# Performance work log

Measured on AMD Instinct MI355X. Metric: run time of the kernel, lower is better.

## Reference

```python
import jax, jax.numpy as jnp
import numpy as np

QLEN, MLEN, BSZ = 1024, 1024, 4
D_MODEL, N_HEAD, D_HEAD, D_INNER = 1024, 16, 64, 4096
KLEN = QLEN + MLEN  # = rlen
LN_EPS = 1e-5


def setup_inputs() -> dict:
    key = jax.random.key(0)
    ks = jax.random.split(key, 16)
    s = 0.02
    nhd = N_HEAD * D_HEAD
    inp = {
        "dec_inp": jax.random.normal(ks[0], (QLEN, BSZ, D_MODEL), jnp.float32),
        "r": jax.random.normal(ks[1], (KLEN, D_MODEL), jnp.float32),
        "r_w_bias": jax.random.normal(ks[2], (N_HEAD, D_HEAD), jnp.float32) * s,
        "r_r_bias": jax.random.normal(ks[3], (N_HEAD, D_HEAD), jnp.float32) * s,
        "mems": jax.random.normal(ks[4], (MLEN, BSZ, D_MODEL), jnp.float32),
        # causal mask with memory: position j visible to query i iff j <= i + MLEN
        "dec_attn_mask": (jnp.arange(KLEN)[None, :] > (jnp.arange(QLEN)[:, None] + MLEN))[:, :, None],
        # parameters
        "qkv_w": jax.random.normal(ks[5], (D_MODEL, 3 * nhd), jnp.float32) * s,
        "r_w": jax.random.normal(ks[6], (D_MODEL, nhd), jnp.float32) * s,
        "o_w": jax.random.normal(ks[7], (nhd, D_MODEL), jnp.float32) * s,
        "ln1_w": jnp.ones((D_MODEL,), jnp.float32),
        "ln1_b": jnp.zeros((D_MODEL,), jnp.float32),
        "ln2_w": jnp.ones((D_MODEL,), jnp.float32),
        "ln2_b": jnp.zeros((D_MODEL,), jnp.float32),
        "ff_w1": jax.random.normal(ks[8], (D_MODEL, D_INNER), jnp.float32) * s,
        "ff_b1": jnp.zeros((D_INNER,), jnp.float32),
        "ff_w2": jax.random.normal(ks[9], (D_INNER, D_MODEL), jnp.float32) * s,
        "ff_b2": jnp.zeros((D_MODEL,), jnp.float32),
    }
    return inp


def _layer_norm(x, w, b):
    mu = jnp.mean(x, axis=-1, keepdims=True)
    var = jnp.mean(jnp.square(x - mu), axis=-1, keepdims=True)
    return (x - mu) * jax.lax.rsqrt(var + LN_EPS) * w + b


def _rel_shift(x):
    # x: [qlen, rlen, bsz, n_head] -- Transformer-XL pad/reshape shift
    q, rl = x.shape[0], x.shape[1]
    zero_pad = jnp.zeros((q, 1) + x.shape[2:], x.dtype)
    x_padded = jnp.concatenate([zero_pad, x], axis=1)
    x_padded = x_padded.reshape((rl + 1, q) + x.shape[2:])
    return x_padded[1:].reshape(x.shape)


def reference(dec_inp, r, r_w_bias, r_r_bias, mems, dec_attn_mask,
              qkv_w, r_w, o_w, ln1_w, ln1_b, ln2_w, ln2_b,
              ff_w1, ff_b1, ff_w2, ff_b2):
    qlen, bsz = dec_inp.shape[0], dec_inp.shape[1]
    nhd = N_HEAD * D_HEAD
    scale = 1.0 / (D_HEAD ** 0.5)

    cat = jnp.concatenate([mems, dec_inp], axis=0)          # [klen, b, d]
    w_heads = cat @ qkv_w                                   # [klen, b, 3*nhd]
    w_head_q, w_head_k, w_head_v = jnp.split(w_heads, 3, axis=-1)
    w_head_q = w_head_q[-qlen:]                             # [qlen, b, nhd]
    klen = w_head_k.shape[0]

    w_head_q = w_head_q.reshape(qlen, bsz, N_HEAD, D_HEAD)
    w_head_k = w_head_k.reshape(klen, bsz, N_HEAD, D_HEAD)
    w_head_v = w_head_v.reshape(klen, bsz, N_HEAD, D_HEAD)
    r_head_k = (r @ r_w).reshape(-1, N_HEAD, D_HEAD)        # [rlen, n, d]

    AC = jnp.einsum('ibnd,jbnd->ijbn', w_head_q + r_w_bias, w_head_k)
    BD = jnp.einsum('ibnd,jnd->ijbn', w_head_q + r_r_bias, r_head_k)
    BD = _rel_shift(BD)

    attn_score = (AC + BD) * scale                          # [q, k, b, n]
    attn_score = jnp.where(dec_attn_mask[:, :, :, None], -jnp.inf, attn_score)
    attn_prob = jax.nn.softmax(attn_score, axis=1)

    attn_vec = jnp.einsum('ijbn,jbnd->ibnd', attn_prob, w_head_v)
    attn_out = attn_vec.reshape(qlen, bsz, nhd) @ o_w       # [q, b, d]

    output = _layer_norm(dec_inp + attn_out, ln1_w, ln1_b)
    ff = jax.nn.relu(output @ ff_w1 + ff_b1) @ ff_w2 + ff_b2
    return _layer_norm(output + ff, ln2_w, ln2_b)
```

## Files before the change

### kernel.cpp

```cpp
#include <hip/hip_runtime.h>
#include <hip/hip_bf16.h>
#include <math.h>

#define QLEN 1024
#define MLEN 1024
#define BSZ 4
#define KLEN 2048
#define NH 16
#define DH 64
#define DM 1024
#define DI 4096
#define NHD 1024
#define LN_EPS 1e-5f

typedef short bf16x8 __attribute__((ext_vector_type(8)));
typedef float f32x4 __attribute__((ext_vector_type(4)));
typedef unsigned int uint4v __attribute__((ext_vector_type(4)));

__device__ __forceinline__ float bf2f(unsigned short u) {
    union { unsigned u32; float f; } x; x.u32 = ((unsigned)u) << 16; return x.f;
}
__device__ __forceinline__ unsigned short f2bf(float f) {
    __hip_bfloat16 h = __float2bfloat16(f);
    return *(unsigned short*)&h;
}

static const size_t OFF_CATB  = 0;
static const size_t OFF_VTG   = 0;
static const size_t OFF_WHB   = 16777216;
static const size_t OFF_RB    = 67108864;
static const size_t OFF_RHKB  = 71303168;
static const size_t OFF_AVB   = 75497472;
static const size_t OFF_TMP   = 83886080;
static const size_t OFF_LN1F  = 100663296;
static const size_t OFF_LN1B  = 117440512;
static const size_t OFF_FFHB  = 125829120;
static const size_t OFF_QKVWT = 159383552;
static const size_t OFF_RWT   = 165675008;
static const size_t OFF_OWT   = 167772160;
static const size_t OFF_FFW1T = 169869312;
static const size_t OFF_FFW2T = 178257920;

__global__ __launch_bounds__(256) void cast_cat(const float* __restrict__ mems,
                                                const float* __restrict__ dec,
                                                unsigned short* __restrict__ out) {
    size_t i8 = ((size_t)blockIdx.x * 256 + threadIdx.x) * 8;
    const size_t half = (size_t)MLEN * BSZ * DM;
    const float* src = (i8 < half) ? (mems + i8) : (dec + (i8 - half));
    float4 v0 = *(const float4*)src;
    float4 v1 = *(const float4*)(src + 4);
    ushort4 o0 = {f2bf(v0.x), f2bf(v0.y), f2bf(v0.z), f2bf(v0.w)};
    ushort4 o1 = {f2bf(v1.x), f2bf(v1.y), f2bf(v1.z), f2bf(v1.w)};
    *(ushort4*)&out[i8] = o0;
    *(ushort4*)&out[i8 + 4] = o1;
}

__global__ __launch_bounds__(256) void cast_f32_bf16(const float* __restrict__ in,
                                                     unsigned short* __restrict__ out) {
    size_t i8 = ((size_t)blockIdx.x * 256 + threadIdx.x) * 8;
    float4 v0 = *(const float4*)(in + i8);
    float4 v1 = *(const float4*)(in + i8 + 4);
    ushort4 o0 = {f2bf(v0.x), f2bf(v0.y), f2bf(v0.z), f2bf(v0.w)};
    ushort4 o1 = {f2bf(v1.x), f2bf(v1.y), f2bf(v1.z), f2bf(v1.w)};
    *(ushort4*)&out[i8] = o0;
    *(ushort4*)&out[i8 + 4] = o1;
}

__global__ __launch_bounds__(256) void transpose_cast_all(
        const float* __restrict__ qkv_w, const float* __restrict__ r_w,
        const float* __restrict__ o_w,  const float* __restrict__ ff_w1,
        const float* __restrict__ ff_w2,
        unsigned short* __restrict__ qkvwT, unsigned short* __restrict__ rwT,
        unsigned short* __restrict__ owT, unsigned short* __restrict__ ffw1T,
        unsigned short* __restrict__ ffw2T) {
    __shared__ float tile[32][33];
    const int bid = blockIdx.x;
    const float* in; unsigned short* out; int K, N, nx, lid;
    if (bid < 3072)      { in = qkv_w; out = qkvwT; K = 1024; N = 3072; nx = 96;  lid = bid; }
    else if (bid < 4096) { in = r_w;   out = rwT;   K = 1024; N = 1024; nx = 32;  lid = bid - 3072; }
    else if (bid < 5120) { in = o_w;   out = owT;   K = 1024; N = 1024; nx = 32;  lid = bid - 4096; }
    else if (bid < 9216) { in = ff_w1; out = ffw1T; K = 1024; N = 4096; nx = 128; lid = bid - 5120; }
    else                 { in = ff_w2; out = ffw2T; K = 4096; N = 1024; nx = 32;  lid = bid - 9216; }
    const int n0 = (lid % nx) * 32;
    const int k0 = (lid / nx) * 32;
    const int t = threadIdx.x;
    const int r = t >> 3;
    const int c0 = (t & 7) << 2;
    float4 v = *(const float4*)&in[(size_t)(k0 + r) * N + n0 + c0];
    tile[r][c0 + 0] = v.x; tile[r][c0 + 1] = v.y;
    tile[r][c0 + 2] = v.z; tile[r][c0 + 3] = v.w;
    __syncthreads();
    ushort4 o = {f2bf(tile[c0 + 0][r]), f2bf(tile[c0 + 1][r]),
                 f2bf(tile[c0 + 2][r]), f2bf(tile[c0 + 3][r])};
    *(ushort4*)&out[(size_t)(n0 + r) * K + k0 + c0] = o;
}

__global__ __launch_bounds__(256) void gemm_bf16(const unsigned short* __restrict__ A,
                                                 const unsigned short* __restrict__ Bt,
                                                 const float* __restrict__ bias,
                                                 void* __restrict__ C,
                                                 int M, int N, int K, int flags) {
    __shared__ __align__(16) unsigned short As[128 * 64];
    __shared__ __align__(16) unsigned short Bs[128 * 64];

    const int tid = threadIdx.x;
    const int w = tid >> 6, l = tid & 63;
    const int wr = w >> 1, wc = w & 1;
    const int row0 = blockIdx.y * 128;
    const int col0 = blockIdx.x * 128;

    f32x4 acc[4][4] = {};

    uint4v ra[4], rb[4];
    {
#pragma unroll
        for (int q = 0; q < 4; ++q) {
            int f = q * 256 + tid, r = f >> 3, c = f & 7;
            ra[q] = *(const uint4v*)&A[(size_t)(row0 + r) * K + c * 8];
            rb[q] = *(const uint4v*)&Bt[(size_t)(col0 + r) * K + c * 8];
        }
    }

    const int nt = K >> 6;
    for (int kt = 0; kt < nt; ++kt) {
        __syncthreads();
#pragma unroll
        for (int q = 0; q < 4; ++q) {
            int f = q * 256 + tid, r = f >> 3, c = f & 7;
            int sw = (c ^ (r & 7)) << 3;
            *(uint4v*)&As[r * 64 + sw] = ra[q];
            *(uint4v*)&Bs[r * 64 + sw] = rb[q];
        }
        __syncthreads();
        if (kt + 1 < nt) {
            const int k0 = (kt + 1) << 6;
#pragma unroll
            for (int q = 0; q < 4; ++q) {
                int f = q * 256 + tid, r = f >> 3, c = f & 7;
                ra[q] = *(const uint4v*)&A[(size_t)(row0 + r) * K + k0 + c * 8];
                rb[q] = *(const uint4v*)&Bt[(size_t)(col0 + r) * K + k0 + c * 8];
            }
        }
#pragma unroll
        for (int ks = 0; ks < 2; ++ks) {
            bf16x8 a[4], bfr[4];
#pragma unroll
            for (int m = 0; m < 4; ++m) {
                int arow = wr * 64 + m * 16 + (l & 15);
                int chunk = (ks * 4 + (l >> 4)) ^ (arow & 7);
                a[m] = *(const bf16x8*)&As[arow * 64 + chunk * 8];
            }
#pragma unroll
            for (int n = 0; n < 4; ++n) {
                int brow = wc * 64 + n * 16 + (l & 15);
                int chunk = (ks * 4 + (l >> 4)) ^ (brow & 7);
                bfr[n] = *(const bf16x8*)&Bs[brow * 64 + chunk * 8];
            }
#pragma unroll
            for (int m = 0; m < 4; ++m)
#pragma unroll
                for (int n = 0; n < 4; ++n)
                    acc[m][n] = __builtin_amdgcn_mfma_f32_16x16x32_bf16(a[m], bfr[n], acc[m][n], 0, 0, 0);
        }
    }

#pragma unroll
    for (int n = 0; n < 4; ++n) {
        const int ccol = col0 + wc * 64 + n * 16 + (l & 15);
        const float bv = (flags & 1) ? bias[ccol] : 0.0f;
#pragma unroll
        for (int m = 0; m < 4; ++m) {
            const int crow0 = row0 + wr * 64 + m * 16 + ((l >> 4) << 2);
#pragma unroll
            for (int reg = 0; reg < 4; ++reg) {
                float v = acc[m][n][reg] + bv;
                if (flags & 2) v = fmaxf(v, 0.0f);
                if (flags & 4)
                    ((unsigned short*)C)[(size_t)(crow0 + reg) * N + ccol] = f2bf(v);
                else
                    ((float*)C)[(size_t)(crow0 + reg) * N + ccol] = v;
            }
        }
    }
}

__global__ __launch_bounds__(256) void vtrans(const unsigned short* __restrict__ whb,
                                              unsigned short* __restrict__ vtg) {
    __shared__ unsigned short tile[64][72];
    const int bn = blockIdx.y;
    const int b = bn >> 4, n = bn & 15, nb = n * 64;
    const int jt0 = blockIdx.x * 64;
    const int tid = threadIdx.x;
#pragma unroll
    for (int g = 0; g < 2; ++g) {
        int f = g * 256 + tid;
        int key = f >> 3, c = f & 7;
        uint4v v = *(const uint4v*)&whb[((size_t)(jt0 + key) * 4 + b) * 3072 + 2048 + nb + c * 8];
        *(uint4v*)&tile[key][c * 8] = v;
    }
    __syncthreads();
#pragma unroll
    for (int g = 0; g < 2; ++g) {
        int f = g * 256 + tid;
        int d = f >> 3, ck = f & 7;
        unsigned short tmp[8];
#pragma unroll
        for (int e = 0; e < 8; ++e) tmp[e] = tile[ck * 8 + e][d];
        *(uint4v*)&vtg[(size_t)bn * 131072 + (size_t)d * 2048 + jt0 + ck * 8] = *(uint4v*)tmp;
    }
}

__global__ __launch_bounds__(512) void flash_attn_mfma(const unsigned short* __restrict__ whb,
                                                       const unsigned short* __restrict__ rhkb,
                                                       const unsigned short* __restrict__ vtg,
                                                       const float* __restrict__ r_w_bias,
                                                       const float* __restrict__ r_r_bias,
                                                       unsigned short* __restrict__ avb) {
    const int bid = blockIdx.x;
    const int bn = bid >> 3;
    const int z = bid & 7;
    const int bx = (z & 1) ? (z >> 1) : 7 - (z >> 1);
    const int b = bn >> 4, n = bn & 15, nb = n * 64;
    const int i0 = bx << 7;
    const int tid = threadIdx.x;
    const int wq = tid >> 6;
    const int lane = tid & 63;
    const int rg = lane >> 4;
    const int lc = lane & 15;
    const int m7 = lc & 7;

    __shared__ __align__(16) unsigned short Ks[4096];
    __shared__ __align__(16) unsigned short Rs[16384];
    __shared__ __align__(16) unsigned short Vt[4096];
    __shared__ __align__(16) unsigned short SCR[8][1408];

    bf16x8 qac0, qac1, qbd0, qbd1;
    {
        const int qrow = MLEN + i0 + wq * 16 + lc;
        const unsigned short* qp = whb + ((size_t)qrow * 4 + b) * 3072 + nb + rg * 8;
        bf16x8 q0 = *(const bf16x8*)(qp);
        bf16x8 q1 = *(const bf16x8*)(qp + 32);
        const float* wbp = r_w_bias + nb + rg * 8;
        const float* rbp = r_r_bias + nb + rg * 8;
#pragma unroll
        for (int e = 0; e < 8; ++e) {
            const float v0 = bf2f((unsigned short)q0[e]);
            const float v1 = bf2f((unsigned short)q1[e]);
            qac0[e] = (short)f2bf((v0 + wbp[e]) * 0.125f);
            qbd0[e] = (short)f2bf((v0 + rbp[e]) * 0.125f);
            qac1[e] = (short)f2bf((v1 + wbp[32 + e]) * 0.125f);
            qbd1[e] = (short)f2bf((v1 + rbp[32 + e]) * 0.125f);
        }
    }

    f32x4 Oacc[4] = {};
    float mrun = -INFINITY, lrun = 0.f;

    const int ntiles = 2 * bx + 18;
    const int wbase_off = 112 - 16 * wq;

    const int srow = tid >> 3;
    const int sc = tid & 7;
    unsigned short* scr = &SCR[wq][0];

    uint4v pk, pv, pr3[3];
    {
        pk = *(const uint4v*)&whb[((size_t)srow * 4 + b) * 3072 + 1024 + nb + sc * 8];
        pv = *(const uint4v*)&vtg[(size_t)bn * 131072 + (size_t)srow * 2048 + sc * 8];
        const int relbase0 = 896 - i0;
#pragma unroll
        for (int p = 0; p < 3; ++p) {
            const int a = relbase0 + p * 64 + srow;
            pr3[p] = *(const uint4v*)&rhkb[(size_t)a * 1024 + nb + sc * 8];
        }
    }

    for (int kt = 0; kt < ntiles; ++kt) {
        const int jt0 = kt << 6;
        const int relbase = jt0 - i0 + 896;
        __syncthreads();

        *(uint4v*)&Ks[srow * 64 + ((sc ^ (srow & 7)) << 3)] = pk;
        *(uint4v*)&Vt[srow * 64 + ((sc ^ (srow & 7)) << 3)] = pv;
        if (kt == 0) {
#pragma unroll
            for (int p = 0; p < 3; ++p) {
                const int a = relbase + p * 64 + srow;
                const int dst = ((a >> 6) & 3) * 4096 + (a & 63) * 64 + ((sc ^ (a & 7)) << 3);
                *(uint4v*)&Rs[dst] = pr3[p];
            }
        } else {
            const int a = relbase + 128 + srow;
            const int dst = ((a >> 6) & 3) * 4096 + (a & 63) * 64 + ((sc ^ (a & 7)) << 3);
            *(uint4v*)&Rs[dst] = pr3[0];
        }
        if (kt + 1 < ntiles) {
            const int jn = jt0 + 64;
            pk = *(const uint4v*)&whb[((size_t)(jn + srow) * 4 + b) * 3072 + 1024 + nb + sc * 8];
            pv = *(const uint4v*)&vtg[(size_t)bn * 131072 + (size_t)srow * 2048 + jn + sc * 8];
            int a = relbase + 192 + srow;
            if (a > 2047) a = 2047;
            pr3[0] = *(const uint4v*)&rhkb[(size_t)a * 1024 + nb + sc * 8];
        }
        __syncthreads();

        f32x4 S[4];
        __builtin_amdgcn_s_setprio(1);
#pragma unroll
        for (int nf = 0; nf < 4; ++nf) {
            const int row = nf * 16 + lc;
            const bf16x8 kf0 = *(const bf16x8*)&Ks[row * 64 + ((rg ^ m7) << 3)];
            const bf16x8 kf1 = *(const bf16x8*)&Ks[row * 64 + (((4 + rg) ^ m7) << 3)];
            f32x4 zz = {0.f, 0.f, 0.f, 0.f};
            zz = __builtin_amdgcn_mfma_f32_16x16x32_bf16(kf0, qac0, zz, 0, 0, 0);
            S[nf] = __builtin_amdgcn_mfma_f32_16x16x32_bf16(kf1, qac1, zz, 0, 0, 0);
        }
        __builtin_amdgcn_s_setprio(0);

        const int wbase = relbase + wbase_off;
#pragma unroll
        for (int g = 0; g < 5; ++g) {
            const int a = wbase + g * 16 + lc;
            const int rbase = ((a >> 6) & 3) * 4096 + (a & 63) * 64;
            const bf16x8 rf0 = *(const bf16x8*)&Rs[rbase + ((rg ^ m7) << 3)];
            const bf16x8 rf1 = *(const bf16x8*)&Rs[rbase + (((4 + rg) ^ m7) << 3)];
            f32x4 bd = {0.f, 0.f, 0.f, 0.f};
            bd = __builtin_amdgcn_mfma_f32_16x16x32_bf16(rf0, qbd0, bd, 0, 0, 0);
            bd = __builtin_amdgcn_mfma_f32_16x16x32_bf16(rf1, qbd1, bd, 0, 0, 0);
            ushort4 p4 = {f2bf(bd[0]), f2bf(bd[1]), f2bf(bd[2]), f2bf(bd[3])};
            *(ushort4*)&scr[lc * 88 + g * 16 + rg * 4] = p4;
        }

        const bool needmask = (wbase + 78 > 2047);
        float tmax = -INFINITY;
#pragma unroll
        for (int nf = 0; nf < 4; ++nf) {
#pragma unroll
            for (int r = 0; r < 4; ++r) {
                const int wb_ = 15 + nf * 16 + rg * 4 + r - lc;
                float s = S[nf][r] + bf2f(scr[lc * 88 + wb_]);
                if (needmask) s = (wbase + wb_ <= 2047) ? s : -INFINITY;
                S[nf][r] = s;
                tmax = fmaxf(tmax, s);
            }
        }

        tmax = fmaxf(tmax, __shfl_xor(tmax, 16));
        tmax = fmaxf(tmax, __shfl_xor(tmax, 32));
        const float mn = fmaxf(mrun, tmax);
        const float ef = __expf(mrun - mn);
        mrun = mn;
        float rsum = 0.f;
#pragma unroll
        for (int nf = 0; nf < 4; ++nf) {
#pragma unroll
            for (int r = 0; r < 4; ++r) {
                const float p = __expf(S[nf][r] - mn);
                S[nf][r] = p;
                rsum += p;
            }
        }
        rsum += __shfl_xor(rsum, 16);
        rsum += __shfl_xor(rsum, 32);
        lrun = lrun * ef + rsum;
        if (__any(ef < 1.0f)) {
#pragma unroll
            for (int nf = 0; nf < 4; ++nf)
#pragma unroll
                for (int r = 0; r < 4; ++r) Oacc[nf][r] *= ef;
        }

#pragma unroll
        for (int nf = 0; nf < 4; ++nf) {
            ushort4 pw = {f2bf(S[nf][0]), f2bf(S[nf][1]), f2bf(S[nf][2]), f2bf(S[nf][3])};
            const int chunk = nf * 2 + (rg >> 1);
            *(ushort4*)&scr[lc * 88 + ((chunk ^ m7) << 3) + ((rg & 1) << 2)] = pw;
        }

        {
            const bf16x8 pf0 = *(const bf16x8*)&scr[lc * 88 + ((rg ^ m7) << 3)];
            const bf16x8 pf1 = *(const bf16x8*)&scr[lc * 88 + (((4 + rg) ^ m7) << 3)];
            __builtin_amdgcn_s_setprio(1);
#pragma unroll
            for (int nf = 0; nf < 4; ++nf) {
                const int row = nf * 16 + lc;
                const bf16x8 vf0 = *(const bf16x8*)&Vt[row * 64 + ((rg ^ m7) << 3)];
                const bf16x8 vf1 = *(const bf16x8*)&Vt[row * 64 + (((4 + rg) ^ m7) << 3)];
                Oacc[nf] = __builtin_amdgcn_mfma_f32_16x16x32_bf16(vf0, pf0, Oacc[nf], 0, 0, 0);
                Oacc[nf] = __builtin_amdgcn_mfma_f32_16x16x32_bf16(vf1, pf1, Oacc[nf], 0, 0, 0);
            }
            __builtin_amdgcn_s_setprio(0);
        }
    }

    const float inv = 1.0f / lrun;
    const int qg = i0 + wq * 16 + lc;
#pragma unroll
    for (int nf = 0; nf < 4; ++nf) {
        ushort4 o = {f2bf(Oacc[nf][0] * inv), f2bf(Oacc[nf][1] * inv),
                     f2bf(Oacc[nf][2] * inv), f2bf(Oacc[nf][3] * inv)};
        *(ushort4*)&avb[((size_t)qg * 4 + b) * 1024 + nb + nf * 16 + rg * 4] = o;
    }
}

__global__ __launch_bounds__(256) void add_ln_kernel(const float* __restrict__ a,
                                                     const float* __restrict__ b,
                                                     const float* __restrict__ w,
                                                     const float* __restrict__ bias,
                                                     float* __restrict__ out,
                                                     unsigned short* __restrict__ out_bf) {
    const int row = blockIdx.x;
    const int t = threadIdx.x;
    const int c0 = t << 2;
    __shared__ float red[256];

    const float4 av = *(const float4*)&a[(size_t)row * DM + c0];
    const float4 bv = *(const float4*)&b[(size_t)row * DM + c0];
    float x0 = av.x + bv.x, x1 = av.y + bv.y, x2 = av.z + bv.z, x3 = av.w + bv.w;

    red[t] = x0 + x1 + x2 + x3;
    __syncthreads();
    for (int off = 128; off > 0; off >>= 1) {
        if (t < off) red[t] += red[t + off];
        __syncthreads();
    }
    const float mu = red[0] * (1.0f / DM);
    __syncthreads();

    const float d0 = x0 - mu, d1 = x1 - mu, d2 = x2 - mu, d3 = x3 - mu;
    red[t] = d0 * d0 + d1 * d1 + d2 * d2 + d3 * d3;
    __syncthreads();
    for (int off = 128; off > 0; off >>= 1) {
        if (t < off) red[t] += red[t + off];
        __syncthreads();
    }
    const float rstd = rsqrtf(red[0] * (1.0f / DM) + LN_EPS);

    const float4 wv = *(const float4*)&w[c0];
    const float4 bsv = *(const float4*)&bias[c0];
    float4 o = {d0 * rstd * wv.x + bsv.x, d1 * rstd * wv.y + bsv.y,
                d2 * rstd * wv.z + bsv.z, d3 * rstd * wv.w + bsv.w};
    *(float4*)&out[(size_t)row * DM + c0] = o;
    if (out_bf) {
        ushort4 ob = {f2bf(o.x), f2bf(o.y), f2bf(o.z), f2bf(o.w)};
        *(ushort4*)&out_bf[(size_t)row * DM + c0] = ob;
    }
}

extern "C" void kernel_launch(void* const* d_in, const int* in_sizes, int n_in,
                              void* d_out, int out_size, void* d_ws, size_t ws_size,
                              hipStream_t stream) {
    const float* dec_inp  = (const float*)d_in[0];
    const float* r        = (const float*)d_in[1];
    const float* r_w_bias = (const float*)d_in[2];
    const float* r_r_bias = (const float*)d_in[3];
    const float* mems     = (const float*)d_in[4];
    const float* qkv_w    = (const float*)d_in[6];
    const float* r_w      = (const float*)d_in[7];
    const float* o_w      = (const float*)d_in[8];
    const float* ln1_w    = (const float*)d_in[9];
    const float* ln1_b    = (const float*)d_in[10];
    const float* ln2_w    = (const float*)d_in[11];
    const float* ln2_b    = (const float*)d_in[12];
    const float* ff_w1    = (const float*)d_in[13];
    const float* ff_b1    = (const float*)d_in[14];
    const float* ff_w2    = (const float*)d_in[15];
    const float* ff_b2    = (const float*)d_in[16];
    float* out = (float*)d_out;
    char* ws = (char*)d_ws;

    unsigned short* catb  = (unsigned short*)(ws + OFF_CATB);
    unsigned short* vtg   = (unsigned short*)(ws + OFF_VTG);
    unsigned short* whb   = (unsigned short*)(ws + OFF_WHB);
    unsigned short* rb    = (unsigned short*)(ws + OFF_RB);
    unsigned short* rhkb  = (unsigned short*)(ws + OFF_RHKB);
    unsigned short* avb   = (unsigned short*)(ws + OFF_AVB);
    float*          tmp   = (float*)(ws + OFF_TMP);
    float*          ln1f  = (float*)(ws + OFF_LN1F);
    unsigned short* ln1b  = (unsigned short*)(ws + OFF_LN1B);
    unsigned short* ffhb  = (unsigned short*)(ws + OFF_FFHB);
    unsigned short* qkvwT = (unsigned short*)(ws + OFF_QKVWT);
    unsigned short* rwT   = (unsigned short*)(ws + OFF_RWT);
    unsigned short* owT   = (unsigned short*)(ws + OFF_OWT);
    unsigned short* ffw1T = (unsigned short*)(ws + OFF_FFW1T);
    unsigned short* ffw2T = (unsigned short*)(ws + OFF_FFW2T);

    cast_cat<<<dim3(4096), 256, 0, stream>>>(mems, dec_inp, catb);
    cast_f32_bf16<<<dim3(1024), 256, 0, stream>>>(r, rb);
    transpose_cast_all<<<dim3(13312), 256, 0, stream>>>(
        qkv_w, r_w, o_w, ff_w1, ff_w2, qkvwT, rwT, owT, ffw1T, ffw2T);

    gemm_bf16<<<dim3(24, 64), 256, 0, stream>>>(catb, qkvwT, nullptr, whb,
                                                KLEN * BSZ, 3 * NHD, DM, 4);
    gemm_bf16<<<dim3(8, 16), 256, 0, stream>>>(rb, rwT, nullptr, rhkb,
                                               KLEN, NHD, DM, 4);

    vtrans<<<dim3(32, 64), 256, 0, stream>>>(whb, vtg);

    flash_attn_mfma<<<dim3(512), 512, 0, stream>>>(
        whb, rhkb, vtg, r_w_bias, r_r_bias, avb);

    gemm_bf16<<<dim3(8, 32), 256, 0, stream>>>(avb, owT, nullptr, tmp,
                                               QLEN * BSZ, DM, NHD, 0);
    add_ln_kernel<<<dim3(QLEN * BSZ), 256, 0, stream>>>(
        dec_inp, tmp, ln1_w, ln1_b, ln1f, ln1b);
    gemm_bf16<<<dim3(32, 32), 256, 0, stream>>>(ln1b, ffw1T, ff_b1, ffhb,
                                                QLEN * BSZ, DI, DM, 1 | 2 | 4);
    gemm_bf16<<<dim3(8, 32), 256, 0, stream>>>(ffhb, ffw2T, ff_b2, tmp,
                                               QLEN * BSZ, DM, DI, 1);
    add_ln_kernel<<<dim3(QLEN * BSZ), 256, 0, stream>>>(
        ln1f, tmp, ln2_w, ln2_b, out, nullptr);
}
```

Measured before the change: 402.8 us.

## Load rel-pos K fragments directly from global and store GEMM outputs as bf16

The attention kernel stops staging the relative-position key tile in shared memory. Each lane now loads its R fragments straight from global memory into registers every tile, which removes the Rs buffer and its LDS traffic and frees shared memory for occupancy. Separately, the o_w and FF2 GEMMs now write bf16 instead of fp32, and the add+LayerNorm kernels read bf16, which halves that intermediate traffic. The cost is redundant global loads of overlapping R rows and lower precision in the residual branch before LayerNorm.

```diff
diff --git a/kernel.cpp b/kernel.cpp
--- a/kernel.cpp
+++ b/kernel.cpp
@@ -31,7 +31,7 @@
 static const size_t OFF_RB    = 67108864;
 static const size_t OFF_RHKB  = 71303168;
 static const size_t OFF_AVB   = 75497472;
-static const size_t OFF_TMP   = 83886080;
+static const size_t OFF_TMPB  = 83886080;
 static const size_t OFF_LN1F  = 100663296;
 static const size_t OFF_LN1B  = 117440512;
 static const size_t OFF_FFHB  = 125829120;
@@ -230,7 +230,6 @@
     const int m7 = lc & 7;
 
     __shared__ __align__(16) unsigned short Ks[4096];
-    __shared__ __align__(16) unsigned short Rs[16384];
     __shared__ __align__(16) unsigned short Vt[4096];
     __shared__ __align__(16) unsigned short SCR[8][1408];
 
@@ -263,44 +262,37 @@
     const int sc = tid & 7;
     unsigned short* scr = &SCR[wq][0];
 
-    uint4v pk, pv, pr3[3];
+    const unsigned short* rfr = rhkb + nb + rg * 8;
+
+    uint4v pk, pv;
     {
         pk = *(const uint4v*)&whb[((size_t)srow * 4 + b) * 3072 + 1024 + nb + sc * 8];
         pv = *(const uint4v*)&vtg[(size_t)bn * 131072 + (size_t)srow * 2048 + sc * 8];
-        const int relbase0 = 896 - i0;
-#pragma unroll
-        for (int p = 0; p < 3; ++p) {
-            const int a = relbase0 + p * 64 + srow;
-            pr3[p] = *(const uint4v*)&rhkb[(size_t)a * 1024 + nb + sc * 8];
-        }
     }
 
     for (int kt = 0; kt < ntiles; ++kt) {
         const int jt0 = kt << 6;
         const int relbase = jt0 - i0 + 896;
+        const int wbase = relbase + wbase_off;
+
+        bf16x8 rfl[5], rfh[5];
+#pragma unroll
+        for (int g = 0; g < 5; ++g) {
+            int a = wbase + g * 16 + lc;
+            if (a > 2047) a = 2047;
+            const unsigned short* rp = rfr + (size_t)a * 1024;
+            rfl[g] = *(const bf16x8*)(rp);
+            rfh[g] = *(const bf16x8*)(rp + 32);
+        }
+
         __syncthreads();
 
         *(uint4v*)&Ks[srow * 64 + ((sc ^ (srow & 7)) << 3)] = pk;
         *(uint4v*)&Vt[srow * 64 + ((sc ^ (srow & 7)) << 3)] = pv;
-        if (kt == 0) {
-#pragma unroll
-            for (int p = 0; p < 3; ++p) {
-                const int a = relbase + p * 64 + srow;
-                const int dst = ((a >> 6) & 3) * 4096 + (a & 63) * 64 + ((sc ^ (a & 7)) << 3);
-                *(uint4v*)&Rs[dst] = pr3[p];
-            }
-        } else {
-            const int a = relbase + 128 + srow;
-            const int dst = ((a >> 6) & 3) * 4096 + (a & 63) * 64 + ((sc ^ (a & 7)) << 3);
-            *(uint4v*)&Rs[dst] = pr3[0];
-        }
         if (kt + 1 < ntiles) {
             const int jn = jt0 + 64;
             pk = *(const uint4v*)&whb[((size_t)(jn + srow) * 4 + b) * 3072 + 1024 + nb + sc * 8];
             pv = *(const uint4v*)&vtg[(size_t)bn * 131072 + (size_t)srow * 2048 + jn + sc * 8];
-            int a = relbase + 192 + srow;
-            if (a > 2047) a = 2047;
-            pr3[0] = *(const uint4v*)&rhkb[(size_t)a * 1024 + nb + sc * 8];
         }
         __syncthreads();
 
@@ -317,16 +309,11 @@
         }
         __builtin_amdgcn_s_setprio(0);
 
-        const int wbase = relbase + wbase_off;
 #pragma unroll
         for (int g = 0; g < 5; ++g) {
-            const int a = wbase + g * 16 + lc;
-            const int rbase = ((a >> 6) & 3) * 4096 + (a & 63) * 64;
-            const bf16x8 rf0 = *(const bf16x8*)&Rs[rbase + ((rg ^ m7) << 3)];
-            const bf16x8 rf1 = *(const bf16x8*)&Rs[rbase + (((4 + rg) ^ m7) << 3)];
             f32x4 bd = {0.f, 0.f, 0.f, 0.f};
-            bd = __builtin_amdgcn_mfma_f32_16x16x32_bf16(rf0, qbd0, bd, 0, 0, 0);
-            bd = __builtin_amdgcn_mfma_f32_16x16x32_bf16(rf1, qbd1, bd, 0, 0, 0);
+            bd = __builtin_amdgcn_mfma_f32_16x16x32_bf16(rfl[g], qbd0, bd, 0, 0, 0);
+            bd = __builtin_amdgcn_mfma_f32_16x16x32_bf16(rfh[g], qbd1, bd, 0, 0, 0);
             ushort4 p4 = {f2bf(bd[0]), f2bf(bd[1]), f2bf(bd[2]), f2bf(bd[3])};
             *(ushort4*)&scr[lc * 88 + g * 16 + rg * 4] = p4;
         }
@@ -404,7 +391,7 @@
 }
 
 __global__ __launch_bounds__(256) void add_ln_kernel(const float* __restrict__ a,
-                                                     const float* __restrict__ b,
+                                                     const unsigned short* __restrict__ b,
                                                      const float* __restrict__ w,
                                                      const float* __restrict__ bias,
                                                      float* __restrict__ out,
@@ -415,8 +402,9 @@
     __shared__ float red[256];
 
     const float4 av = *(const float4*)&a[(size_t)row * DM + c0];
-    const float4 bv = *(const float4*)&b[(size_t)row * DM + c0];
-    float x0 = av.x + bv.x, x1 = av.y + bv.y, x2 = av.z + bv.z, x3 = av.w + bv.w;
+    const ushort4 bu = *(const ushort4*)&b[(size_t)row * DM + c0];
+    float x0 = av.x + bf2f(bu.x), x1 = av.y + bf2f(bu.y);
+    float x2 = av.z + bf2f(bu.z), x3 = av.w + bf2f(bu.w);
 
     red[t] = x0 + x1 + x2 + x3;
     __syncthreads();
@@ -475,7 +463,7 @@
     unsigned short* rb    = (unsigned short*)(ws + OFF_RB);
     unsigned short* rhkb  = (unsigned short*)(ws + OFF_RHKB);
     unsigned short* avb   = (unsigned short*)(ws + OFF_AVB);
-    float*          tmp   = (float*)(ws + OFF_TMP);
+    unsigned short* tmpb  = (unsigned short*)(ws + OFF_TMPB);
     float*          ln1f  = (float*)(ws + OFF_LN1F);
     unsigned short* ln1b  = (unsigned short*)(ws + OFF_LN1B);
     unsigned short* ffhb  = (unsigned short*)(ws + OFF_FFHB);
@@ -500,14 +488,14 @@
     flash_attn_mfma<<<dim3(512), 512, 0, stream>>>(
         whb, rhkb, vtg, r_w_bias, r_r_bias, avb);
 
-    gemm_bf16<<<dim3(8, 32), 256, 0, stream>>>(avb, owT, nullptr, tmp,
-                                               QLEN * BSZ, DM, NHD, 0);
+    gemm_bf16<<<dim3(8, 32), 256, 0, stream>>>(avb, owT, nullptr, tmpb,
+                                               QLEN * BSZ, DM, NHD, 4);
     add_ln_kernel<<<dim3(QLEN * BSZ), 256, 0, stream>>>(
-        dec_inp, tmp, ln1_w, ln1_b, ln1f, ln1b);
+        dec_inp, tmpb, ln1_w, ln1_b, ln1f, ln1b);
     gemm_bf16<<<dim3(32, 32), 256, 0, stream>>>(ln1b, ffw1T, ff_b1, ffhb,
                                                 QLEN * BSZ, DI, DM, 1 | 2 | 4);
-    gemm_bf16<<<dim3(8, 32), 256, 0, stream>>>(ffhb, ffw2T, ff_b2, tmp,
-                                               QLEN * BSZ, DM, DI, 1);
+    gemm_bf16<<<dim3(8, 32), 256, 0, stream>>>(ffhb, ffw2T, ff_b2, tmpb,
+                                               QLEN * BSZ, DM, DI, 1 | 4);
     add_ln_kernel<<<dim3(QLEN * BSZ), 256, 0, stream>>>(
-        ln1f, tmp, ln2_w, ln2_b, out, nullptr);
-}
+        ln1f, tmpb, ln2_w, ln2_b, out, nullptr);
+}
```

Result: slower. 498.6 us (+23.8%).
